# Kernel optimization log

Measured on AMD Instinct MI355X. Metric: run time of the kernel, lower is better.

Reference implementation:

```python
import jax, jax.numpy as jnp
import numpy as np

B, T, P, H, LAT = 64, 256, 128, 512, 128


def _run_lstm(x, Wih, Whh, b, h0, c0):
    """Single unidirectional LSTM layer, PyTorch gate order (i,f,g,o).
    x: (B,T,in) -> outputs (B,T,H), final h (B,H)."""
    xW = jnp.einsum('bti,gi->btg', x, Wih) + b  # precompute input projection (B,T,4H)

    def step(carry, xw_t):
        h, c = carry
        g = xw_t + h @ Whh.T
        i, f, gg, o = jnp.split(g, 4, axis=-1)
        c = jax.nn.sigmoid(f) * c + jax.nn.sigmoid(i) * jnp.tanh(gg)
        h = jax.nn.sigmoid(o) * jnp.tanh(c)
        return (h, c), h

    (hT, cT), hs = jax.lax.scan(step, (h0, c0), jnp.swapaxes(xW, 0, 1))
    return jnp.swapaxes(hs, 0, 1), hT


def setup_inputs() -> dict:
    key = jax.random.key(0)
    ks = iter(jax.random.split(key, 40))
    rn = lambda shape, s=0.05: jax.random.normal(next(ks), shape, jnp.float32) * s
    inp = {
        'x': (jax.random.uniform(next(ks), (B, T, P)) < 0.1).astype(jnp.float32),
        'e0f_Wih': rn((4 * H, P)), 'e0f_Whh': rn((4 * H, H)), 'e0f_b': jnp.zeros((4 * H,), jnp.float32),
        'e0b_Wih': rn((4 * H, P)), 'e0b_Whh': rn((4 * H, H)), 'e0b_b': jnp.zeros((4 * H,), jnp.float32),
        'e1f_Wih': rn((4 * H, 2 * H)), 'e1f_Whh': rn((4 * H, H)), 'e1f_b': jnp.zeros((4 * H,), jnp.float32),
        'e1b_Wih': rn((4 * H, 2 * H)), 'e1b_Whh': rn((4 * H, H)), 'e1b_b': jnp.zeros((4 * H,), jnp.float32),
        'enc_fc_W': rn((LAT, 2 * H)), 'enc_fc_b': jnp.zeros((LAT,), jnp.float32),
        'dec_fc_W': rn((H, LAT)), 'dec_fc_b': jnp.zeros((H,), jnp.float32),
        'start_token': rn((1, 1, P), 0.1),
        'd0_Wih': rn((4 * H, P)), 'd0_Whh': rn((4 * H, H)), 'd0_b': jnp.zeros((4 * H,), jnp.float32),
        'd1_Wih': rn((4 * H, H)), 'd1_Whh': rn((4 * H, H)), 'd1_b': jnp.zeros((4 * H,), jnp.float32),
        'out_W': rn((P, H)), 'out_b': jnp.zeros((P,), jnp.float32),
        'teacher_forcing_ratio': 1,
    }
    return inp


def reference(x, e0f_Wih, e0f_Whh, e0f_b, e0b_Wih, e0b_Whh, e0b_b,
              e1f_Wih, e1f_Whh, e1f_b, e1b_Wih, e1b_Whh, e1b_b,
              enc_fc_W, enc_fc_b, dec_fc_W, dec_fc_b, start_token,
              d0_Wih, d0_Whh, d0_b, d1_Wih, d1_Whh, d1_b, out_W, out_b,
              teacher_forcing_ratio):
    b = x.shape[0]
    z0 = jnp.zeros((b, H), x.dtype)
    # ---- encoder: 2-layer bidirectional LSTM ----
    f0, _ = _run_lstm(x, e0f_Wih, e0f_Whh, e0f_b, z0, z0)
    r0, _ = _run_lstm(x[:, ::-1], e0b_Wih, e0b_Whh, e0b_b, z0, z0)
    l0 = jnp.concatenate([f0, r0[:, ::-1]], axis=-1)  # (B,T,2H)
    _, h_fwd = _run_lstm(l0, e1f_Wih, e1f_Whh, e1f_b, z0, z0)
    _, h_bwd = _run_lstm(l0[:, ::-1], e1b_Wih, e1b_Whh, e1b_b, z0, z0)
    z = jnp.concatenate([h_fwd, h_bwd], axis=-1) @ enc_fc_W.T + enc_fc_b  # (B,LAT)
    # ---- decoder: teacher-forced 2-layer LSTM ----
    h0d = z @ dec_fc_W.T + dec_fc_b  # (B,H), repeated for every layer
    xs = jnp.concatenate([jnp.broadcast_to(start_token, (b, 1, P)), x[:, :-1]], axis=1)
    o0, _ = _run_lstm(xs, d0_Wih, d0_Whh, d0_b, h0d, z0)
    o1, _ = _run_lstm(o0, d1_Wih, d1_Whh, d1_b, h0d, z0)
    x_hat = jax.nn.sigmoid(o1 @ out_W.T + out_b)  # (B,T,P)
    return x_hat, z
```

## Files before the change

kernel.cpp:

```cpp
#include <hip/hip_runtime.h>
#include <stdint.h>


typedef unsigned short u16;
typedef unsigned int u32;
typedef float f32x4 __attribute__((ext_vector_type(4)));
typedef __bf16 bf16x8 __attribute__((ext_vector_type(8)));
typedef unsigned int u32x4 __attribute__((ext_vector_type(4)));

#define AT_LD(p) __hip_atomic_load((p), __ATOMIC_RELAXED, __HIP_MEMORY_SCOPE_AGENT)
#define AT_ST(p, v) __hip_atomic_store((p), (v), __ATOMIC_RELAXED, __HIP_MEMORY_SCOPE_AGENT)

__device__ __forceinline__ u16 f2bf(float f) {
  u32 u = __builtin_bit_cast(u32, f);
  u += 0x7FFFu + ((u >> 16) & 1u);
  return (u16)(u >> 16);
}
__device__ __forceinline__ float bf2f(u16 h) {
  return __builtin_bit_cast(float, (u32)h << 16);
}
__device__ __forceinline__ bf16x8 ld8(const u16* p) {
  u32x4 v = *(const u32x4*)p;
  return __builtin_bit_cast(bf16x8, v);
}
__device__ __forceinline__ float sigf(float x) { return 1.f / (1.f + __expf(-x)); }
__device__ __forceinline__ float tanhx(float x) {
  x = fminf(fmaxf(x, -15.f), 15.f);
  float e = __expf(2.f * x);
  return (e - 1.f) / (e + 1.f);
}

__global__ void k_prep_x(const float* __restrict__ x, const float* __restrict__ st,
                         u16* __restrict__ Ax, u16* __restrict__ Axs, int n) {
  int i = blockIdx.x * 256 + threadIdx.x;
  if (i >= n) return;
  Ax[i] = f2bf(x[i]);
  int col = i & 127;
  int t = (i >> 7) & 255;
  float v = (t == 0) ? st[col] : x[i - 128];
  Axs[i] = f2bf(v);
}

__global__ void k_cvt(const float* __restrict__ in, u16* __restrict__ out, int n) {
  int i = blockIdx.x * 256 + threadIdx.x;
  if (i < n) out[i] = f2bf(in[i]);
}

__global__ __launch_bounds__(256) void k_gemm_bt(
    const u16* __restrict__ A, const u16* __restrict__ B, const float* __restrict__ bias,
    u16* __restrict__ Cb, float* __restrict__ Cf, int M, int N, int K, int sig) {
  __shared__ __align__(16) u16 As[128 * 64];
  __shared__ __align__(16) u16 Bs[128 * 64];
  const int m0 = blockIdx.x * 128, n0 = blockIdx.y * 128;
  const int tid = threadIdx.x, lane = tid & 63, wave = tid >> 6;
  const int wm = wave >> 1, wn = wave & 1;

  f32x4 acc[4][4];
#pragma unroll
  for (int i = 0; i < 4; ++i)
#pragma unroll
    for (int j = 0; j < 4; ++j) acc[i][j] = (f32x4){0.f, 0.f, 0.f, 0.f};

  const int nkt = K >> 6;
  for (int kt = 0; kt < nkt; ++kt) {
#pragma unroll
    for (int i = 0; i < 4; ++i) {
      int ch = tid + (i << 8);
      int row = ch >> 3, k8 = ch & 7;
      int dst = row * 128 + ((k8 * 16) ^ ((row & 7) << 4));
      u32x4 va = *(const u32x4*)(A + (size_t)(m0 + row) * K + kt * 64 + k8 * 8);
      *(u32x4*)((char*)As + dst) = va;
      u32x4 vb = *(const u32x4*)(B + (size_t)(n0 + row) * K + kt * 64 + k8 * 8);
      *(u32x4*)((char*)Bs + dst) = vb;
    }
    __syncthreads();
#pragma unroll
    for (int kk = 0; kk < 2; ++kk) {
      int kb = kk * 64 + ((lane >> 4) << 4);
      bf16x8 afr[4], bfr[4];
#pragma unroll
      for (int i = 0; i < 4; ++i) {
        int ra = wm * 64 + i * 16 + (lane & 15);
        afr[i] = ld8((const u16*)((const char*)As + ra * 128 + (kb ^ ((ra & 7) << 4))));
        int rb = wn * 64 + i * 16 + (lane & 15);
        bfr[i] = ld8((const u16*)((const char*)Bs + rb * 128 + (kb ^ ((rb & 7) << 4))));
      }
#pragma unroll
      for (int i = 0; i < 4; ++i)
#pragma unroll
        for (int j = 0; j < 4; ++j)
          acc[i][j] = __builtin_amdgcn_mfma_f32_16x16x32_bf16(afr[i], bfr[j], acc[i][j], 0, 0, 0);
    }
    __syncthreads();
  }
#pragma unroll
  for (int i = 0; i < 4; ++i) {
#pragma unroll
    for (int j = 0; j < 4; ++j) {
      int col = n0 + wn * 64 + j * 16 + (lane & 15);
      float bv = bias ? bias[col] : 0.f;
#pragma unroll
      for (int r = 0; r < 4; ++r) {
        int row = m0 + wm * 64 + i * 16 + ((lane >> 4) << 2) + r;
        float v = acc[i][j][r] + bv;
        if (sig) Cf[(size_t)row * N + col] = 1.f / (1.f + __expf(-v));
        else     Cb[(size_t)row * N + col] = f2bf(v);
      }
    }
  }
}

struct Rec2 {
  const u16* xW[8];
  const u16* Whh[8];
  const u16* Wih[8];
  const float* bias[8];
  const float* h0[8];
  u16* seq[8];
  float* hfin[8];
  u16* hxc[8];
  int prod[8];
  int seqstride[8]; int coloff[8]; int rev[8]; int hfinstride[8];
  int grp[8]; int fused[8]; int fullp[8];
  u32* tags;
};

__global__ __launch_bounds__(256, 1) void k_rec2(Rec2 p) {
  const int chain = blockIdx.x & 7;
  const int c = blockIdx.x >> 3;
  const int tid = threadIdx.x, lane = tid & 63, wave = tid >> 6;
  const int arow = lane & 15, kg = lane >> 4;

  const u16* __restrict__ xW = p.xW[chain];
  const u16* __restrict__ Whh = p.Whh[chain];
  const u16* __restrict__ Wih = p.Wih[chain];
  const float* __restrict__ bias = p.bias[chain];
  const float* __restrict__ h0 = p.h0[chain];
  u16* seq = p.seq[chain];
  float* hfin = p.hfin[chain];
  u32* hx = (u32*)p.hxc[chain];
  const u32* hxp = (const u32*)p.hxc[p.prod[chain]];
  const int grp = p.grp[chain], rev = p.rev[chain];
  const int fused = p.fused[chain], fullp = p.fullp[chain];
  const int sstride = p.seqstride[chain], coloff = p.coloff[chain];
  const int hstride = p.hfinstride[chain];
  u32* myt = p.tags + chain * 64;
  const u32* pt = p.tags + p.prod[chain] * 64;

  __shared__ __align__(16) u16 Wlds[64][64][8];
  __shared__ __align__(16) u16 Xlds[64][64][8];
  __shared__ __align__(16) u16 hbufA[8192];
  __shared__ float gbuf[4][16][16];
  __shared__ float cbuf[256];
  __shared__ float bbuf[64];

  for (int e = tid; e < 4096; e += 256) {
    int n = e >> 6, k8 = e & 63;
    int grow = ((n >> 4) << 9) + (c << 4) + (n & 15);
    *(u32x4*)(&Wlds[k8][n][0]) = *(const u32x4*)(Whh + (size_t)grow * 512 + k8 * 8);
    if (fused)
      *(u32x4*)(&Xlds[k8][n][0]) = *(const u32x4*)(Wih + (size_t)grow * 512 + k8 * 8);
  }
  if (tid < 64) bbuf[tid] = fused ? bias[((tid >> 4) << 9) + (c << 4) + (tid & 15)] : 0.f;
  cbuf[tid] = 0.f;
  if (tid < 128) {
    int row = tid >> 3, q = tid & 7;
    float a = 0.f, b2 = 0.f;
    if (h0) {
      a = h0[(size_t)(grp * 16 + row) * 512 + (c << 4) + 2 * q];
      b2 = h0[(size_t)(grp * 16 + row) * 512 + (c << 4) + 2 * q + 1];
    }
    u32 pk = (u32)f2bf(a) | ((u32)f2bf(b2) << 16);
    AT_ST(hx + (size_t)c * 128 + (row << 3) + q, pk);
  }
  asm volatile("s_waitcnt vmcnt(0)" ::: "memory");
  __syncthreads();
  if (tid == 0) AT_ST(myt + c, 1u);

  for (int t = 0; t < 256; ++t) {
    const int t_eff = rev ? 255 - t : t;
    const int slot = fullp ? t : (t & 3);
    const int slotn = fullp ? (t + 1) : ((t + 1) & 3);

    float xwv[4] = {0.f, 0.f, 0.f, 0.f};
    if (!fused) {
#pragma unroll
      for (int r4 = 0; r4 < 4; ++r4) {
        int row = (kg << 2) + r4;
        xwv[r4] = bf2f(xW[(((size_t)((grp * 16 + row) * 256 + t_eff)) << 11) +
                          (wave << 9) + (c << 4) + arow]);
      }
    }
    if (wave == 0) {
      u32 thr_own = (u32)(t + 1), thr_prod = (u32)(t + 2);
      while (true) {
        int ok = 1;
        if (lane < 32) {
          if (lane != c) ok = (AT_LD(myt + lane) >= thr_own);
        } else if (fused) {
          ok = (AT_LD(pt + (lane - 32)) >= thr_prod);
        }
        if (__all(ok)) break;
        __builtin_amdgcn_s_sleep(1);
      }
    }
    __syncthreads();
    __builtin_amdgcn_sched_barrier(0);

#pragma unroll
    for (int i = 0; i < 4; ++i) {
      int cid = tid + (i << 8);
      int row = cid >> 6, ch8 = cid & 63;
      const u32* src = hx + ((size_t)slot * 32 + (ch8 >> 1)) * 128 +
                       (row << 3) + ((ch8 & 1) << 2);
      u32x4 v;
      v.x = AT_LD(src + 0); v.y = AT_LD(src + 1);
      v.z = AT_LD(src + 2); v.w = AT_LD(src + 3);
      *(u32x4*)((char*)hbufA + row * 1024 + ((ch8 << 4) ^ ((row & 7) << 4))) = v;
    }
    bf16x8 xf[16];
    if (fused) {
#pragma unroll
      for (int kt = 0; kt < 16; ++kt) {
        const u32* hp = hxp + ((size_t)(t + 1) * 32 + 2 * kt + (kg >> 1)) * 128 +
                        (arow << 3) + ((kg & 1) << 2);
        u32x4 v;
        v.x = AT_LD(hp + 0); v.y = AT_LD(hp + 1);
        v.z = AT_LD(hp + 2); v.w = AT_LD(hp + 3);
        xf[kt] = __builtin_bit_cast(bf16x8, v);
      }
    }
    __syncthreads();

    bf16x8 af[16];
#pragma unroll
    for (int kt = 0; kt < 16; ++kt)
      af[kt] = ld8((const u16*)((const char*)hbufA + arow * 1024 +
                                ((kt * 64 + (kg << 4)) ^ ((arow & 7) << 4))));
    f32x4 ae = {0.f, 0.f, 0.f, 0.f}, ao = {0.f, 0.f, 0.f, 0.f};
#pragma unroll
    for (int kt = 0; kt < 16; ++kt) {
      bf16x8 bw = ld8(&Wlds[(kt << 2) + kg][(wave << 4) + arow][0]);
      if (kt & 1) ao = __builtin_amdgcn_mfma_f32_16x16x32_bf16(af[kt], bw, ao, 0, 0, 0);
      else        ae = __builtin_amdgcn_mfma_f32_16x16x32_bf16(af[kt], bw, ae, 0, 0, 0);
      if (fused) {
        bf16x8 bx = ld8(&Xlds[(kt << 2) + kg][(wave << 4) + arow][0]);
        if (kt & 1) ae = __builtin_amdgcn_mfma_f32_16x16x32_bf16(xf[kt], bx, ae, 0, 0, 0);
        else        ao = __builtin_amdgcn_mfma_f32_16x16x32_bf16(xf[kt], bx, ao, 0, 0, 0);
      }
    }
#pragma unroll
    for (int r4 = 0; r4 < 4; ++r4)
      gbuf[wave][(kg << 2) + r4][arow] = ae[r4] + ao[r4] + xwv[r4];
    __syncthreads();

    u32 pk = 0; int row2 = 0, j0 = 0;
    float hh0 = 0.f, hh1 = 0.f;
    if (tid >= 128) {
      int t2 = tid - 128;
      row2 = t2 >> 3; int q = t2 & 7; j0 = q << 1;
      float i0 = gbuf[0][row2][j0], i1 = gbuf[0][row2][j0 + 1];
      float f0 = gbuf[1][row2][j0], f1 = gbuf[1][row2][j0 + 1];
      float g0 = gbuf[2][row2][j0], g1 = gbuf[2][row2][j0 + 1];
      float o0v = gbuf[3][row2][j0], o1v = gbuf[3][row2][j0 + 1];
      if (fused) {
        i0 += bbuf[j0]; i1 += bbuf[j0 + 1];
        f0 += bbuf[16 + j0]; f1 += bbuf[16 + j0 + 1];
        g0 += bbuf[32 + j0]; g1 += bbuf[32 + j0 + 1];
        o0v += bbuf[48 + j0]; o1v += bbuf[48 + j0 + 1];
      }
      int ci = (row2 << 4) + j0;
      float cc0 = sigf(f0) * cbuf[ci] + sigf(i0) * tanhx(g0);
      float cc1 = sigf(f1) * cbuf[ci + 1] + sigf(i1) * tanhx(g1);
      cbuf[ci] = cc0; cbuf[ci + 1] = cc1;
      hh0 = sigf(o0v) * tanhx(cc0);
      hh1 = sigf(o1v) * tanhx(cc1);
      pk = (u32)f2bf(hh0) | ((u32)f2bf(hh1) << 16);
      AT_ST(hx + ((size_t)slotn * 32 + c) * 128 + (row2 << 3) + q, pk);
      asm volatile("s_waitcnt vmcnt(0)" ::: "memory");
    }
    __syncthreads();
    if (tid == 128) AT_ST(myt + c, (u32)(t + 2));
    if (tid >= 128) {
      if (seq)
        *(u32*)(seq + ((size_t)((grp * 16 + row2) * 256 + t_eff)) * sstride +
                coloff + (c << 4) + j0) = pk;
      if (hfin && t == 255) {
        hfin[(size_t)(grp * 16 + row2) * hstride + (c << 4) + j0] = hh0;
        hfin[(size_t)(grp * 16 + row2) * hstride + (c << 4) + j0 + 1] = hh1;
      }
    }
  }
}

__global__ void k_enc_head(const float* __restrict__ hcat, const float* __restrict__ W,
                           const float* __restrict__ b, float* __restrict__ zws,
                           float* __restrict__ zout) {
  int bi = blockIdx.x, j = threadIdx.x;
  const float* h = hcat + bi * 1024;
  const float* w = W + j * 1024;
  float s = b[j];
  for (int k = 0; k < 1024; ++k) s += h[k] * w[k];
  zws[bi * 128 + j] = s;
  zout[bi * 128 + j] = s;
}

__global__ void k_dec_head(const float* __restrict__ z, const float* __restrict__ W,
                           const float* __restrict__ b, float* __restrict__ h0d) {
  int bi = blockIdx.x, j = threadIdx.x;
  const float* zz = z + bi * 128;
  const float* w = W + j * 128;
  float s = b[j];
  for (int k = 0; k < 128; ++k) s += zz[k] * w[k];
  h0d[bi * 512 + j] = s;
}

extern "C" void kernel_launch(void* const* d_in, const int* in_sizes, int n_in,
                              void* d_out, int out_size, void* d_ws, size_t ws_size,
                              hipStream_t stream) {
  (void)in_sizes; (void)n_in; (void)out_size;
  const float* x        = (const float*)d_in[0];
  const float* e0f_Wih  = (const float*)d_in[1];
  const float* e0f_Whh  = (const float*)d_in[2];
  const float* e0f_b    = (const float*)d_in[3];
  const float* e0b_Wih  = (const float*)d_in[4];
  const float* e0b_Whh  = (const float*)d_in[5];
  const float* e0b_b    = (const float*)d_in[6];
  const float* e1f_Wih  = (const float*)d_in[7];
  const float* e1f_Whh  = (const float*)d_in[8];
  const float* e1f_b    = (const float*)d_in[9];
  const float* e1b_Wih  = (const float*)d_in[10];
  const float* e1b_Whh  = (const float*)d_in[11];
  const float* e1b_b    = (const float*)d_in[12];
  const float* enc_fc_W = (const float*)d_in[13];
  const float* enc_fc_b = (const float*)d_in[14];
  const float* dec_fc_W = (const float*)d_in[15];
  const float* dec_fc_b = (const float*)d_in[16];
  const float* start_tk = (const float*)d_in[17];
  const float* d0_Wih   = (const float*)d_in[18];
  const float* d0_Whh   = (const float*)d_in[19];
  const float* d0_b     = (const float*)d_in[20];
  const float* d1_Wih   = (const float*)d_in[21];
  const float* d1_Whh   = (const float*)d_in[22];
  const float* d1_b     = (const float*)d_in[23];
  const float* out_W    = (const float*)d_in[24];
  const float* out_b    = (const float*)d_in[25];

  uintptr_t base = (uintptr_t)d_ws;
  size_t off = 0;
  auto carve = [&](size_t bytes) -> void* {
    off = (off + 255) & ~(size_t)255;
    void* p = (void*)(base + off);
    off += bytes;
    return p;
  };
  u16* Ax     = (u16*)carve((size_t)2097152 * 2);
  u16* Axs    = (u16*)carve((size_t)2097152 * 2);
  u16* Wb_e0f = (u16*)carve((size_t)262144 * 2);
  u16* Wb_e0b = (u16*)carve((size_t)262144 * 2);
  u16* Wb_d0  = (u16*)carve((size_t)262144 * 2);
  u16* Wb_e1f = (u16*)carve((size_t)2097152 * 2);
  u16* Wb_e1b = (u16*)carve((size_t)2097152 * 2);
  u16* Wb_d1  = (u16*)carve((size_t)1048576 * 2);
  u16* Wb_out = (u16*)carve((size_t)65536 * 2);
  u16* Wh_e0f = (u16*)carve((size_t)1048576 * 2);
  u16* Wh_e0b = (u16*)carve((size_t)1048576 * 2);
  u16* Wh_e1f = (u16*)carve((size_t)1048576 * 2);
  u16* Wh_e1b = (u16*)carve((size_t)1048576 * 2);
  u16* Wh_d0  = (u16*)carve((size_t)1048576 * 2);
  u16* Wh_d1  = (u16*)carve((size_t)1048576 * 2);
  u16* slot0  = (u16*)carve((size_t)16384 * 2048 * 2);
  u16* slot1  = (u16*)carve((size_t)16384 * 2048 * 2);
  u16* l0     = (u16*)carve((size_t)33619968);
  u16* hxring = (u16*)carve((size_t)524288);
  float* hcat = (float*)carve((size_t)65536 * 4);
  float* zws  = (float*)carve((size_t)8192 * 4);
  float* h0d  = (float*)carve((size_t)32768 * 4);
  u32* tags0  = (u32*)carve(2048);
  u32* tags1  = (u32*)carve(2048);
  u32* tags2  = (u32*)carve(2048);
  if (off > ws_size) return;

  u16* o1     = l0;
  u16* hxprod = l0 + 8388608;

  (void)hipMemsetAsync(tags0, 0, 6144, stream);

  k_prep_x<<<8192, 256, 0, stream>>>(x, start_tk, Ax, Axs, 2097152);
  k_cvt<<<1024, 256, 0, stream>>>(e0f_Wih, Wb_e0f, 262144);
  k_cvt<<<1024, 256, 0, stream>>>(e0b_Wih, Wb_e0b, 262144);
  k_cvt<<<1024, 256, 0, stream>>>(d0_Wih, Wb_d0, 262144);
  k_cvt<<<8192, 256, 0, stream>>>(e1f_Wih, Wb_e1f, 2097152);
  k_cvt<<<8192, 256, 0, stream>>>(e1b_Wih, Wb_e1b, 2097152);
  k_cvt<<<4096, 256, 0, stream>>>(d1_Wih, Wb_d1, 1048576);
  k_cvt<<<256, 256, 0, stream>>>(out_W, Wb_out, 65536);
  k_cvt<<<4096, 256, 0, stream>>>(e0f_Whh, Wh_e0f, 1048576);
  k_cvt<<<4096, 256, 0, stream>>>(e0b_Whh, Wh_e0b, 1048576);
  k_cvt<<<4096, 256, 0, stream>>>(e1f_Whh, Wh_e1f, 1048576);
  k_cvt<<<4096, 256, 0, stream>>>(e1b_Whh, Wh_e1b, 1048576);
  k_cvt<<<4096, 256, 0, stream>>>(d0_Whh, Wh_d0, 1048576);
  k_cvt<<<4096, 256, 0, stream>>>(d1_Whh, Wh_d1, 1048576);

  k_gemm_bt<<<dim3(128, 16), 256, 0, stream>>>(Ax, Wb_e0f, e0f_b, slot0, nullptr, 16384, 2048, 128, 0);
  k_gemm_bt<<<dim3(128, 16), 256, 0, stream>>>(Ax, Wb_e0b, e0b_b, slot1, nullptr, 16384, 2048, 128, 0);
  {
    Rec2 r{};
    for (int ch = 0; ch < 8; ++ch) {
      int dir2 = ch >> 2, g = ch & 3;
      r.xW[ch] = dir2 ? slot1 : slot0;
      r.Whh[ch] = dir2 ? Wh_e0b : Wh_e0f;
      r.Wih[ch] = nullptr; r.bias[ch] = nullptr; r.h0[ch] = nullptr;
      r.seq[ch] = l0; r.seqstride[ch] = 1024; r.coloff[ch] = dir2 ? 512 : 0;
      r.rev[ch] = dir2; r.hfin[ch] = nullptr; r.hfinstride[ch] = 0;
      r.grp[ch] = g; r.fused[ch] = 0; r.fullp[ch] = 0; r.prod[ch] = 0;
      r.hxc[ch] = hxring + (size_t)ch * 32768;
    }
    r.tags = tags0;
    k_rec2<<<256, 256, 0, stream>>>(r);
  }
  k_gemm_bt<<<dim3(128, 16), 256, 0, stream>>>(l0, Wb_e1f, e1f_b, slot0, nullptr, 16384, 2048, 1024, 0);
  k_gemm_bt<<<dim3(128, 16), 256, 0, stream>>>(l0, Wb_e1b, e1b_b, slot1, nullptr, 16384, 2048, 1024, 0);
  {
    Rec2 r{};
    for (int ch = 0; ch < 8; ++ch) {
      int dir2 = ch >> 2, g = ch & 3;
      r.xW[ch] = dir2 ? slot1 : slot0;
      r.Whh[ch] = dir2 ? Wh_e1b : Wh_e1f;
      r.Wih[ch] = nullptr; r.bias[ch] = nullptr; r.h0[ch] = nullptr;
      r.seq[ch] = nullptr; r.seqstride[ch] = 0; r.coloff[ch] = 0;
      r.rev[ch] = dir2; r.hfin[ch] = hcat + (dir2 ? 512 : 0); r.hfinstride[ch] = 1024;
      r.grp[ch] = g; r.fused[ch] = 0; r.fullp[ch] = 0; r.prod[ch] = 0;
      r.hxc[ch] = hxring + (size_t)ch * 32768;
    }
    r.tags = tags1;
    k_rec2<<<256, 256, 0, stream>>>(r);
  }
  k_enc_head<<<64, 128, 0, stream>>>(hcat, enc_fc_W, enc_fc_b, zws, ((float*)d_out) + 2097152);
  k_dec_head<<<64, 512, 0, stream>>>(zws, dec_fc_W, dec_fc_b, h0d);
  k_gemm_bt<<<dim3(128, 16), 256, 0, stream>>>(Axs, Wb_d0, d0_b, slot0, nullptr, 16384, 2048, 128, 0);
  {
    Rec2 r{};
    for (int ch = 0; ch < 4; ++ch) {
      r.xW[ch] = slot0;
      r.Whh[ch] = Wh_d0;
      r.Wih[ch] = nullptr; r.bias[ch] = nullptr; r.h0[ch] = h0d;
      r.seq[ch] = nullptr; r.seqstride[ch] = 0; r.coloff[ch] = 0;
      r.rev[ch] = 0; r.hfin[ch] = nullptr; r.hfinstride[ch] = 0;
      r.grp[ch] = ch; r.fused[ch] = 0; r.fullp[ch] = 1; r.prod[ch] = 0;
      r.hxc[ch] = hxprod + (size_t)ch * 2105344;
    }
    for (int ch = 4; ch < 8; ++ch) {
      r.xW[ch] = nullptr;
      r.Whh[ch] = Wh_d1;
      r.Wih[ch] = Wb_d1; r.bias[ch] = d1_b; r.h0[ch] = h0d;
      r.seq[ch] = o1; r.seqstride[ch] = 512; r.coloff[ch] = 0;
      r.rev[ch] = 0; r.hfin[ch] = nullptr; r.hfinstride[ch] = 0;
      r.grp[ch] = ch - 4; r.fused[ch] = 1; r.fullp[ch] = 0; r.prod[ch] = ch - 4;
      r.hxc[ch] = hxring + (size_t)ch * 32768;
    }
    r.tags = tags2;
    k_rec2<<<256, 256, 0, stream>>>(r);
  }
  k_gemm_bt<<<dim3(128, 1), 256, 0, stream>>>(o1, Wb_out, out_b, nullptr, (float*)d_out, 16384, 128, 512, 1);
}
```

Before: 5.518 ms.

## Interleave gate columns so each wave computes LSTM cell in registers

Reorders the recurrent weight rows so that i/f/g/o gates for the same hidden unit land in adjacent lanes of one wave. The cell update then runs in registers via shuffles instead of going through an LDS gate buffer, which removes two block barriers per timestep. Each wave publishes its own progress tag, so consumers poll 128 tags instead of 32. The LDS weight layout is XOR-swizzled to avoid bank conflicts. The 13 weight-conversion launches are also merged into one kernel. Per-wave tags add polling traffic, and the shuffle-based gate exchange must be exactly right for correctness.

After: 5.689 ms. +3.1%, slower.

```diff
diff --git a/kernel.cpp b/kernel.cpp
--- a/kernel.cpp
+++ b/kernel.cpp
@@ -41,9 +41,19 @@
   Axs[i] = f2bf(v);
 }
 
-__global__ void k_cvt(const float* __restrict__ in, u16* __restrict__ out, int n) {
+struct CvtJobs {
+  const float* src[13];
+  u16* dst[13];
+  int off[14];
+};
+__global__ void k_cvt_all(CvtJobs j, int total) {
   int i = blockIdx.x * 256 + threadIdx.x;
-  if (i < n) out[i] = f2bf(in[i]);
+  if (i >= total) return;
+  int a = 0;
+#pragma unroll
+  for (int k = 1; k < 13; ++k) a += (i >= j.off[k]) ? 1 : 0;
+  int local = i - j.off[a];
+  j.dst[a][local] = f2bf(j.src[a][local]);
 }
 
 __global__ __launch_bounds__(256) void k_gemm_bt(
@@ -110,7 +120,7 @@
   }
 }
 
-struct Rec2 {
+struct Rec3 {
   const u16* xW[8];
   const u16* Whh[8];
   const u16* Wih[8];
@@ -125,11 +135,15 @@
   u32* tags;
 };
 
-__global__ __launch_bounds__(256, 1) void k_rec2(Rec2 p) {
+__global__ __launch_bounds__(256, 1) void k_rec3(Rec3 p) {
   const int chain = blockIdx.x & 7;
   const int c = blockIdx.x >> 3;
   const int tid = threadIdx.x, lane = tid & 63, wave = tid >> 6;
   const int arow = lane & 15, kg = lane >> 4;
+  const int g4 = arow & 3;
+  const int h4 = arow >> 2;
+  const int myrow = (kg << 2) + g4;
+  const int mycol = (wave << 2) + h4;
 
   const u16* __restrict__ xW = p.xW[chain];
   const u16* __restrict__ Whh = p.Whh[chain];
@@ -144,38 +158,36 @@
   const int fused = p.fused[chain], fullp = p.fullp[chain];
   const int sstride = p.seqstride[chain], coloff = p.coloff[chain];
   const int hstride = p.hfinstride[chain];
-  u32* myt = p.tags + chain * 64;
-  const u32* pt = p.tags + p.prod[chain] * 64;
+  u32* myt = p.tags + chain * 128;
+  const u32* pt = p.tags + p.prod[chain] * 128;
 
   __shared__ __align__(16) u16 Wlds[64][64][8];
   __shared__ __align__(16) u16 Xlds[64][64][8];
   __shared__ __align__(16) u16 hbufA[8192];
-  __shared__ float gbuf[4][16][16];
-  __shared__ float cbuf[256];
   __shared__ float bbuf[64];
 
   for (int e = tid; e < 4096; e += 256) {
     int n = e >> 6, k8 = e & 63;
-    int grow = ((n >> 4) << 9) + (c << 4) + (n & 15);
-    *(u32x4*)(&Wlds[k8][n][0]) = *(const u32x4*)(Whh + (size_t)grow * 512 + k8 * 8);
+    int grow = ((n & 3) << 9) + (c << 4) + (n >> 2);
+    int ns = n ^ (k8 & 3);
+    *(u32x4*)(&Wlds[k8][ns][0]) = *(const u32x4*)(Whh + (size_t)grow * 512 + k8 * 8);
     if (fused)
-      *(u32x4*)(&Xlds[k8][n][0]) = *(const u32x4*)(Wih + (size_t)grow * 512 + k8 * 8);
-  }
-  if (tid < 64) bbuf[tid] = fused ? bias[((tid >> 4) << 9) + (c << 4) + (tid & 15)] : 0.f;
-  cbuf[tid] = 0.f;
-  if (tid < 128) {
-    int row = tid >> 3, q = tid & 7;
-    float a = 0.f, b2 = 0.f;
-    if (h0) {
-      a = h0[(size_t)(grp * 16 + row) * 512 + (c << 4) + 2 * q];
-      b2 = h0[(size_t)(grp * 16 + row) * 512 + (c << 4) + 2 * q + 1];
-    }
-    u32 pk = (u32)f2bf(a) | ((u32)f2bf(b2) << 16);
-    AT_ST(hx + (size_t)c * 128 + (row << 3) + q, pk);
+      *(u32x4*)(&Xlds[k8][ns][0]) = *(const u32x4*)(Wih + (size_t)grow * 512 + k8 * 8);
+  }
+  if (tid < 64) bbuf[tid] = fused ? bias[((tid & 3) << 9) + (c << 4) + (tid >> 2)] : 0.f;
+
+  float creg = 0.f;
+
+  {
+    float hv = h0 ? h0[(size_t)(grp * 16 + myrow) * 512 + (c << 4) + mycol] : 0.f;
+    u32 mypk = (u32)f2bf(hv);
+    u32 part = (u32)__shfl_xor((int)mypk, 4);
+    if ((h4 & 1) == 0)
+      AT_ST(hx + ((size_t)0 * 32 + c) * 128 + (myrow << 3) + (mycol >> 1), mypk | (part << 16));
   }
   asm volatile("s_waitcnt vmcnt(0)" ::: "memory");
+  if (lane == 0) AT_ST(myt + c * 4 + wave, 1u);
   __syncthreads();
-  if (tid == 0) AT_ST(myt + c, 1u);
 
   for (int t = 0; t < 256; ++t) {
     const int t_eff = rev ? 255 - t : t;
@@ -185,27 +197,22 @@
     float xwv[4] = {0.f, 0.f, 0.f, 0.f};
     if (!fused) {
 #pragma unroll
-      for (int r4 = 0; r4 < 4; ++r4) {
-        int row = (kg << 2) + r4;
-        xwv[r4] = bf2f(xW[(((size_t)((grp * 16 + row) * 256 + t_eff)) << 11) +
-                          (wave << 9) + (c << 4) + arow]);
+      for (int r = 0; r < 4; ++r) {
+        int row = (kg << 2) + r;
+        xwv[r] = bf2f(xW[((size_t)((grp * 16 + row) * 256 + t_eff)) * 2048 +
+                         (g4 << 9) + (c << 4) + mycol]);
       }
     }
     if (wave == 0) {
-      u32 thr_own = (u32)(t + 1), thr_prod = (u32)(t + 2);
+      u32 to = (u32)(t + 1), tp = (u32)(t + 2);
       while (true) {
-        int ok = 1;
-        if (lane < 32) {
-          if (lane != c) ok = (AT_LD(myt + lane) >= thr_own);
-        } else if (fused) {
-          ok = (AT_LD(pt + (lane - 32)) >= thr_prod);
-        }
+        int ok = (AT_LD(myt + lane) >= to) & (AT_LD(myt + 64 + lane) >= to);
+        if (fused) ok &= (AT_LD(pt + lane) >= tp) & (AT_LD(pt + 64 + lane) >= tp);
         if (__all(ok)) break;
         __builtin_amdgcn_s_sleep(1);
       }
     }
     __syncthreads();
-    __builtin_amdgcn_sched_barrier(0);
 
 #pragma unroll
     for (int i = 0; i < 4; ++i) {
@@ -238,58 +245,61 @@
       af[kt] = ld8((const u16*)((const char*)hbufA + arow * 1024 +
                                 ((kt * 64 + (kg << 4)) ^ ((arow & 7) << 4))));
     f32x4 ae = {0.f, 0.f, 0.f, 0.f}, ao = {0.f, 0.f, 0.f, 0.f};
+    const int nswz = (wave << 4) + arow;
 #pragma unroll
     for (int kt = 0; kt < 16; ++kt) {
-      bf16x8 bw = ld8(&Wlds[(kt << 2) + kg][(wave << 4) + arow][0]);
+      bf16x8 bw = ld8(&Wlds[(kt << 2) + kg][nswz ^ kg][0]);
       if (kt & 1) ao = __builtin_amdgcn_mfma_f32_16x16x32_bf16(af[kt], bw, ao, 0, 0, 0);
       else        ae = __builtin_amdgcn_mfma_f32_16x16x32_bf16(af[kt], bw, ae, 0, 0, 0);
       if (fused) {
-        bf16x8 bx = ld8(&Xlds[(kt << 2) + kg][(wave << 4) + arow][0]);
+        bf16x8 bx = ld8(&Xlds[(kt << 2) + kg][nswz ^ kg][0]);
         if (kt & 1) ae = __builtin_amdgcn_mfma_f32_16x16x32_bf16(xf[kt], bx, ae, 0, 0, 0);
         else        ao = __builtin_amdgcn_mfma_f32_16x16x32_bf16(xf[kt], bx, ao, 0, 0, 0);
       }
     }
-#pragma unroll
-    for (int r4 = 0; r4 < 4; ++r4)
-      gbuf[wave][(kg << 2) + r4][arow] = ae[r4] + ao[r4] + xwv[r4];
-    __syncthreads();
-
-    u32 pk = 0; int row2 = 0, j0 = 0;
-    float hh0 = 0.f, hh1 = 0.f;
-    if (tid >= 128) {
-      int t2 = tid - 128;
-      row2 = t2 >> 3; int q = t2 & 7; j0 = q << 1;
-      float i0 = gbuf[0][row2][j0], i1 = gbuf[0][row2][j0 + 1];
-      float f0 = gbuf[1][row2][j0], f1 = gbuf[1][row2][j0 + 1];
-      float g0 = gbuf[2][row2][j0], g1 = gbuf[2][row2][j0 + 1];
-      float o0v = gbuf[3][row2][j0], o1v = gbuf[3][row2][j0 + 1];
-      if (fused) {
-        i0 += bbuf[j0]; i1 += bbuf[j0 + 1];
-        f0 += bbuf[16 + j0]; f1 += bbuf[16 + j0 + 1];
-        g0 += bbuf[32 + j0]; g1 += bbuf[32 + j0 + 1];
-        o0v += bbuf[48 + j0]; o1v += bbuf[48 + j0 + 1];
-      }
-      int ci = (row2 << 4) + j0;
-      float cc0 = sigf(f0) * cbuf[ci] + sigf(i0) * tanhx(g0);
-      float cc1 = sigf(f1) * cbuf[ci + 1] + sigf(i1) * tanhx(g1);
-      cbuf[ci] = cc0; cbuf[ci + 1] = cc1;
-      hh0 = sigf(o0v) * tanhx(cc0);
-      hh1 = sigf(o1v) * tanhx(cc1);
-      pk = (u32)f2bf(hh0) | ((u32)f2bf(hh1) << 16);
-      AT_ST(hx + ((size_t)slotn * 32 + c) * 128 + (row2 << 3) + q, pk);
-      asm volatile("s_waitcnt vmcnt(0)" ::: "memory");
-    }
-    __syncthreads();
-    if (tid == 128) AT_ST(myt + c, (u32)(t + 2));
-    if (tid >= 128) {
-      if (seq)
-        *(u32*)(seq + ((size_t)((grp * 16 + row2) * 256 + t_eff)) * sstride +
-                coloff + (c << 4) + j0) = pk;
-      if (hfin && t == 255) {
-        hfin[(size_t)(grp * 16 + row2) * hstride + (c << 4) + j0] = hh0;
-        hfin[(size_t)(grp * 16 + row2) * hstride + (c << 4) + j0 + 1] = hh1;
-      }
-    }
+    float bb = bbuf[nswz];
+    float a0 = ae[0] + ao[0] + xwv[0] + bb;
+    float a1 = ae[1] + ao[1] + xwv[1] + bb;
+    float a2 = ae[2] + ao[2] + xwv[2] + bb;
+    float a3 = ae[3] + ao[3] + xwv[3] + bb;
+
+    float b0, b1, b2, b3;
+    {
+      float s0 = __shfl_xor(a0, 1), s1 = __shfl_xor(a1, 1);
+      float s2 = __shfl_xor(a2, 1), s3 = __shfl_xor(a3, 1);
+      bool j0 = (lane & 1) != 0;
+      b0 = j0 ? s1 : a0;
+      b1 = j0 ? a1 : s0;
+      b2 = j0 ? s3 : a2;
+      b3 = j0 ? a3 : s2;
+    }
+    float iv, fv, gv, ov;
+    {
+      float u0 = __shfl_xor(b0, 2), u1 = __shfl_xor(b1, 2);
+      float u2 = __shfl_xor(b2, 2), u3 = __shfl_xor(b3, 2);
+      bool j1 = (lane & 2) != 0;
+      iv = j1 ? u2 : b0;
+      fv = j1 ? u3 : b1;
+      gv = j1 ? b2 : u0;
+      ov = j1 ? b3 : u1;
+    }
+    float cc = sigf(fv) * creg + sigf(iv) * tanhx(gv);
+    creg = cc;
+    float hh = sigf(ov) * tanhx(cc);
+
+    u32 mypk = (u32)f2bf(hh);
+    u32 part = (u32)__shfl_xor((int)mypk, 4);
+    u32 pk = mypk | (part << 16);
+    bool evenh = ((h4 & 1) == 0);
+    if (evenh)
+      AT_ST(hx + ((size_t)slotn * 32 + c) * 128 + (myrow << 3) + (mycol >> 1), pk);
+    asm volatile("s_waitcnt vmcnt(0)" ::: "memory");
+    if (lane == 0) AT_ST(myt + c * 4 + wave, (u32)(t + 2));
+    if (seq && evenh)
+      *(u32*)(seq + ((size_t)((grp * 16 + myrow) * 256 + t_eff)) * sstride +
+              coloff + (c << 4) + mycol) = pk;
+    if (hfin && t == 255)
+      hfin[(size_t)(grp * 16 + myrow) * hstride + (c << 4) + mycol] = hh;
   }
 }
 
@@ -376,35 +386,35 @@
   float* hcat = (float*)carve((size_t)65536 * 4);
   float* zws  = (float*)carve((size_t)8192 * 4);
   float* h0d  = (float*)carve((size_t)32768 * 4);
-  u32* tags0  = (u32*)carve(2048);
-  u32* tags1  = (u32*)carve(2048);
-  u32* tags2  = (u32*)carve(2048);
+  u32* tags0  = (u32*)carve(4096);
+  u32* tags1  = (u32*)carve(4096);
+  u32* tags2  = (u32*)carve(4096);
   if (off > ws_size) return;
 
   u16* o1     = l0;
   u16* hxprod = l0 + 8388608;
 
-  (void)hipMemsetAsync(tags0, 0, 6144, stream);
+  (void)hipMemsetAsync(tags0, 0, 12288, stream);
 
   k_prep_x<<<8192, 256, 0, stream>>>(x, start_tk, Ax, Axs, 2097152);
-  k_cvt<<<1024, 256, 0, stream>>>(e0f_Wih, Wb_e0f, 262144);
-  k_cvt<<<1024, 256, 0, stream>>>(e0b_Wih, Wb_e0b, 262144);
-  k_cvt<<<1024, 256, 0, stream>>>(d0_Wih, Wb_d0, 262144);
-  k_cvt<<<8192, 256, 0, stream>>>(e1f_Wih, Wb_e1f, 2097152);
-  k_cvt<<<8192, 256, 0, stream>>>(e1b_Wih, Wb_e1b, 2097152);
-  k_cvt<<<4096, 256, 0, stream>>>(d1_Wih, Wb_d1, 1048576);
-  k_cvt<<<256, 256, 0, stream>>>(out_W, Wb_out, 65536);
-  k_cvt<<<4096, 256, 0, stream>>>(e0f_Whh, Wh_e0f, 1048576);
-  k_cvt<<<4096, 256, 0, stream>>>(e0b_Whh, Wh_e0b, 1048576);
-  k_cvt<<<4096, 256, 0, stream>>>(e1f_Whh, Wh_e1f, 1048576);
-  k_cvt<<<4096, 256, 0, stream>>>(e1b_Whh, Wh_e1b, 1048576);
-  k_cvt<<<4096, 256, 0, stream>>>(d0_Whh, Wh_d0, 1048576);
-  k_cvt<<<4096, 256, 0, stream>>>(d1_Whh, Wh_d1, 1048576);
+  {
+    CvtJobs j{};
+    const float* s[13] = {e0f_Wih, e0b_Wih, d0_Wih, e1f_Wih, e1b_Wih, d1_Wih, out_W,
+                          e0f_Whh, e0b_Whh, e1f_Whh, e1b_Whh, d0_Whh, d1_Whh};
+    u16* d[13] = {Wb_e0f, Wb_e0b, Wb_d0, Wb_e1f, Wb_e1b, Wb_d1, Wb_out,
+                  Wh_e0f, Wh_e0b, Wh_e1f, Wh_e1b, Wh_d0, Wh_d1};
+    int n[13] = {262144, 262144, 262144, 2097152, 2097152, 1048576, 65536,
+                 1048576, 1048576, 1048576, 1048576, 1048576, 1048576};
+    int acc = 0;
+    for (int k = 0; k < 13; ++k) { j.src[k] = s[k]; j.dst[k] = d[k]; j.off[k] = acc; acc += n[k]; }
+    j.off[13] = acc;
+    k_cvt_all<<<(acc + 255) / 256, 256, 0, stream>>>(j, acc);
+  }
 
   k_gemm_bt<<<dim3(128, 16), 256, 0, stream>>>(Ax, Wb_e0f, e0f_b, slot0, nullptr, 16384, 2048, 128, 0);
   k_gemm_bt<<<dim3(128, 16), 256, 0, stream>>>(Ax, Wb_e0b, e0b_b, slot1, nullptr, 16384, 2048, 128, 0);
   {
-    Rec2 r{};
+    Rec3 r{};
     for (int ch = 0; ch < 8; ++ch) {
       int dir2 = ch >> 2, g = ch & 3;
       r.xW[ch] = dir2 ? slot1 : slot0;
@@ -416,12 +426,12 @@
       r.hxc[ch] = hxring + (size_t)ch * 32768;
     }
     r.tags = tags0;
-    k_rec2<<<256, 256, 0, stream>>>(r);
+    k_rec3<<<256, 256, 0, stream>>>(r);
   }
   k_gemm_bt<<<dim3(128, 16), 256, 0, stream>>>(l0, Wb_e1f, e1f_b, slot0, nullptr, 16384, 2048, 1024, 0);
   k_gemm_bt<<<dim3(128, 16), 256, 0, stream>>>(l0, Wb_e1b, e1b_b, slot1, nullptr, 16384, 2048, 1024, 0);
   {
-    Rec2 r{};
+    Rec3 r{};
     for (int ch = 0; ch < 8; ++ch) {
       int dir2 = ch >> 2, g = ch & 3;
       r.xW[ch] = dir2 ? slot1 : slot0;
@@ -433,13 +443,13 @@
       r.hxc[ch] = hxring + (size_t)ch * 32768;
     }
     r.tags = tags1;
-    k_rec2<<<256, 256, 0, stream>>>(r);
+    k_rec3<<<256, 256, 0, stream>>>(r);
   }
   k_enc_head<<<64, 128, 0, stream>>>(hcat, enc_fc_W, enc_fc_b, zws, ((float*)d_out) + 2097152);
   k_dec_head<<<64, 512, 0, stream>>>(zws, dec_fc_W, dec_fc_b, h0d);
   k_gemm_bt<<<dim3(128, 16), 256, 0, stream>>>(Axs, Wb_d0, d0_b, slot0, nullptr, 16384, 2048, 128, 0);
   {
-    Rec2 r{};
+    Rec3 r{};
     for (int ch = 0; ch < 4; ++ch) {
       r.xW[ch] = slot0;
       r.Whh[ch] = Wh_d0;
@@ -459,7 +469,7 @@
       r.hxc[ch] = hxring + (size_t)ch * 32768;
     }
     r.tags = tags2;
-    k_rec2<<<256, 256, 0, stream>>>(r);
+    k_rec3<<<256, 256, 0, stream>>>(r);
   }
   k_gemm_bt<<<dim3(128, 1), 256, 0, stream>>>(o1, Wb_out, out_b, nullptr, (float*)d_out, 16384, 128, 512, 1);
 }
```
